# Performance work log

Hardware: AMD Instinct MI355X
Metric: run time of the kernel (lower is better)

The kernel has to match this reference:

```python
import jax, jax.numpy as jnp
import numpy as np


def setup_inputs() -> dict:
    key = jax.random.key(0)
    ks = jax.random.split(key, 6)
    bs, T, F, HS, da, r = 64, 512, 128, 256, 64, 8
    s = 0.05  # xavier-ish scale, keeps gates out of saturation
    return {
        "x": jax.random.normal(ks[0], (bs, T, F), jnp.float32),
        "w_first": jax.random.normal(ks[1], (da, F), jnp.float32) * s,
        "b_first": jnp.zeros((da,), jnp.float32),
        "w_second": jax.random.normal(ks[2], (r, da), jnp.float32) * s,
        "b_second": jnp.zeros((r,), jnp.float32),
        "weight_iBarh": jax.random.normal(ks[3], (F, 4 * HS), jnp.float32) * s,
        "weight_hh": jax.random.normal(ks[4], (HS, 4 * HS), jnp.float32) * s,
        "bias": jnp.zeros((4 * HS,), jnp.float32),
    }


def reference(x, w_first, b_first, w_second, b_second, weight_iBarh, weight_hh, bias):
    bs, T, F = x.shape
    HS = weight_hh.shape[0]
    r = w_second.shape[0]
    # attention scores are a fixed per-position function of x -> precompute once
    scores = jnp.tanh(x @ w_first.T + b_first) @ w_second.T + b_second  # [bs, T, r]
    neg = jnp.finfo(x.dtype).min
    t_idx = jnp.arange(T)

    def step(carry, t):
        h, c = carry
        # growing-window softmax over time axis: positions 0..t
        mask = (t_idx <= t)[None, :, None]  # [1, T, 1]
        attn = jax.nn.softmax(jnp.where(mask, scores, neg), axis=1)  # [bs, T, r]
        # matrixM: attention^T @ pastTimeSteps, summed over r heads / r
        M = jnp.einsum('btr,btf->bf', attn, x) / r  # [bs, F]
        gates = M @ weight_iBarh + h @ weight_hh + bias  # [bs, 4*HS]
        i = jax.nn.sigmoid(gates[:, :HS])
        f = jax.nn.sigmoid(gates[:, HS:2 * HS])
        g = jnp.tanh(gates[:, 2 * HS:3 * HS])
        o = jax.nn.sigmoid(gates[:, 3 * HS:])
        c = f * c + i * g
        h = o * jnp.tanh(c)
        return (h, c), h

    h0 = jnp.zeros((bs, HS), x.dtype)
    c0 = jnp.zeros((bs, HS), x.dtype)
    (h_t, c_t), hs = jax.lax.scan(step, (h0, c0), t_idx)
    hidden_seq = jnp.transpose(hs, (1, 0, 2))  # [bs, T, HS]
    # attention returned by the torch code is from the LAST step (full window)
    attention = jnp.transpose(jax.nn.softmax(scores, axis=1), (0, 2, 1))  # [bs, r, T]
    return hidden_seq, h_t, c_t, attention
```

## Files before the change

### kernel.cpp

```cpp
#include <hip/hip_runtime.h>
#include <cmath>

#define T_LEN 512
#define BS    64
#define F_DIM 128
#define HSZ   256
#define DA    64
#define RH    8

#define OFF_HT   8388608
#define OFF_CT   8404992
#define OFF_ATT  8421376

__global__ __launch_bounds__(256) void k_scores(
    const float* __restrict__ x, const float* __restrict__ w1,
    const float* __restrict__ b1, const float* __restrict__ w2,
    const float* __restrict__ b2, float* __restrict__ scores)
{
  __shared__ float wl[DA * 129];
  __shared__ float xs[4][F_DIM];
  __shared__ float hid[4][DA];
  int tid = threadIdx.x;
  for (int id = tid; id < DA * F_DIM; id += 256) {
    int a = id >> 7, f = id & 127;
    wl[a * 129 + f] = w1[id];
  }
  int wv = tid >> 6, lane = tid & 63;
  int pair = blockIdx.x * 4 + wv;
  const float* xr = x + (size_t)pair * F_DIM;
  xs[wv][lane]      = xr[lane];
  xs[wv][64 + lane] = xr[64 + lane];
  __syncthreads();
  float acc = b1[lane];
  #pragma unroll 8
  for (int f = 0; f < F_DIM; ++f)
    acc += xs[wv][f] * wl[lane * 129 + f];
  hid[wv][lane] = tanhf(acc);
  __syncthreads();
  if (lane < RH) {
    float sc = b2[lane];
    #pragma unroll 8
    for (int a = 0; a < DA; ++a)
      sc += hid[wv][a] * w2[lane * DA + a];
    scores[(size_t)pair * RH + lane] = sc;
  }
}

__global__ __launch_bounds__(512) void k_attn_M(
    const float* __restrict__ x, const float* __restrict__ scores,
    float* __restrict__ M, float* __restrict__ out)
{
  __shared__ float se[T_LEN * 9];
  __shared__ float ivd[T_LEN * 9];
  __shared__ float segsum[RH][65];
  __shared__ float cp[4 * F_DIM * RH];
  __shared__ float gmax[RH];
  int tid = threadIdx.x;
  int blk = blockIdx.x;
  int j = blk >> 6, b = blk & 63;
  int p0 = j * 128, e = p0 + 128;
  int e8 = e * 8;
  const float* sb = scores + (size_t)b * T_LEN * RH;
  for (int id = tid; id < e8; id += 512)
    se[(id >> 3) * 9 + (id & 7)] = sb[id];
  __syncthreads();
  {
    int w = tid >> 6, l = tid & 63;
    float m = -INFINITY;
    for (int t = l; t < e; t += 64)
      m = fmaxf(m, se[t * 9 + w]);
    #pragma unroll
    for (int off = 32; off; off >>= 1)
      m = fmaxf(m, __shfl_xor(m, off));
    if (l == 0) gmax[w] = m;
  }
  __syncthreads();
  for (int id = tid; id < e8; id += 512) {
    int t = id >> 3, r = id & 7;
    se[t * 9 + r] = expf(se[t * 9 + r] - gmax[r]);
  }
  __syncthreads();
  int nseg = e >> 3;
  {
    int r = tid >> 6, seg = tid & 63;
    if (seg < nseg) {
      float run = 0.f;
      #pragma unroll
      for (int i = 0; i < 8; ++i) {
        int t = seg * 8 + i;
        run += se[t * 9 + r];
        ivd[t * 9 + r] = run;
      }
      segsum[r][seg] = run;
    }
  }
  __syncthreads();
  if (tid < RH) {
    float off = 0.f;
    for (int sg = 0; sg < nseg; ++sg) {
      float tmp = segsum[tid][sg];
      segsum[tid][sg] = off;
      off += tmp;
    }
  }
  __syncthreads();
  for (int id = tid; id < e8; id += 512) {
    int t = id >> 3, r = id & 7;
    ivd[t * 9 + r] = 1.f / (ivd[t * 9 + r] + segsum[r][t >> 3]);
  }
  __syncthreads();
  if (j == 3) {
    for (int id = tid; id < T_LEN * RH; id += 512) {
      int r = id >> 9, t = id & 511;
      out[OFF_ATT + ((size_t)b * RH + r) * T_LEN + t] =
          se[t * 9 + r] * ivd[511 * 9 + r];
    }
  }
  const float* xb = x + (size_t)b * T_LEN * F_DIM;
  {
    int q = tid >> 7, f = tid & 127;
    int len = p0 >> 2;
    int t0 = q * len, t1 = t0 + len;
    float pp[RH];
    #pragma unroll
    for (int r = 0; r < RH; ++r) pp[r] = 0.f;
    for (int t = t0; t < t1; ++t) {
      float xv = xb[t * F_DIM + f];
      #pragma unroll
      for (int r = 0; r < RH; ++r) pp[r] += se[t * 9 + r] * xv;
    }
    float* c = &cp[(q * F_DIM + f) * RH];
    #pragma unroll
    for (int r = 0; r < RH; ++r) c[r] = pp[r];
  }
  __syncthreads();
  if (tid < F_DIM) {
    int f = tid;
    float num[RH];
    #pragma unroll
    for (int r = 0; r < RH; ++r) num[r] = 0.f;
    #pragma unroll
    for (int q = 0; q < 4; ++q) {
      const float* c = &cp[(q * F_DIM + f) * RH];
      #pragma unroll
      for (int r = 0; r < RH; ++r) num[r] += c[r];
    }
    float* Mb = M + (size_t)b * T_LEN * F_DIM;
    for (int t = p0; t < e; ++t) {
      float xv = xb[t * F_DIM + f];
      float acc = 0.f;
      #pragma unroll
      for (int r = 0; r < RH; ++r) {
        num[r] += se[t * 9 + r] * xv;
        acc += num[r] * ivd[t * 9 + r];
      }
      Mb[t * F_DIM + f] = 0.125f * acc;
    }
  }
}

__global__ __launch_bounds__(1024, 4) void k_lstm(
    const float* __restrict__ M, const float* __restrict__ Wi,
    const float* __restrict__ Wh, const float* __restrict__ bias,
    unsigned long long* __restrict__ slab64,
    float* __restrict__ out)
{
  __shared__ float v[HSZ];
  __shared__ float mst[F_DIM];
  __shared__ float part[1024];
  int tid = threadIdx.x;
  int blk = blockIdx.x;
  int s = blk >> 6;
  int b = blk & 63;
  int kq = tid >> 8;
  int ct = tid & 255;
  int type = ct >> 6, jj = ct & 63;
  int col = type * 256 + s * 64 + jj;

  float w[96];
  #pragma unroll
  for (int k = 0; k < 96; ++k) {
    int kk = kq * 96 + k;
    w[k] = (kk < F_DIM) ? Wi[(size_t)kk * 1024 + col]
                        : Wh[(size_t)(kk - F_DIM) * 1024 + col];
  }
  float bsum = (kq == 0) ? bias[col] : 0.f;
  float c_reg = 0.f;

  if (tid < HSZ) v[tid] = 0.f;
  if (tid >= 512 && tid < 512 + F_DIM)
    mst[tid - 512] = M[(size_t)b * T_LEN * F_DIM + (tid - 512)];
  __syncthreads();

  int pidx = tid >> 6;
  int sp = pidx + (pidx >= s);
  int pj = tid & 63;

  for (int t = 0; t < T_LEN; ++t) {
    float acc = bsum;
    if (kq == 0) {
      #pragma unroll
      for (int k = 0; k < 96; ++k) acc += mst[k] * w[k];
    } else if (kq == 1) {
      #pragma unroll
      for (int k = 0; k < 32; ++k) acc += mst[96 + k] * w[k];
      #pragma unroll
      for (int k = 32; k < 96; ++k) acc += v[k - 32] * w[k];
    } else if (kq == 2) {
      #pragma unroll
      for (int k = 0; k < 96; ++k) acc += v[64 + k] * w[k];
    } else {
      #pragma unroll
      for (int k = 0; k < 96; ++k) acc += v[160 + k] * w[k];
    }
    part[tid] = acc;
    __syncthreads();

    if (tid < 64) {
      float gi = part[tid]       + part[256 + tid] + part[512 + tid] + part[768 + tid];
      float gf = part[64 + tid]  + part[320 + tid] + part[576 + tid] + part[832 + tid];
      float gg = part[128 + tid] + part[384 + tid] + part[640 + tid] + part[896 + tid];
      float go = part[192 + tid] + part[448 + tid] + part[704 + tid] + part[960 + tid];
      float ii = 1.f / (1.f + __expf(-gi));
      float ff = 1.f / (1.f + __expf(-gf));
      float gt = 1.f - 2.f / (__expf(2.f * gg) + 1.f);
      float oo = 1.f / (1.f + __expf(-go));
      c_reg = ff * c_reg + ii * gt;
      float tc = 1.f - 2.f / (__expf(2.f * c_reg) + 1.f);
      float h = oo * tc;
      int hsx = s * 64 + tid;
      v[hsx] = h;
      unsigned long long pk =
          ((unsigned long long)(unsigned)(t + 1) << 32) |
          (unsigned long long)__float_as_uint(h);
      __hip_atomic_store(&slab64[(((t & 1) * BS + b) * 4 + s) * 64 + tid], pk,
                         __ATOMIC_RELAXED, __HIP_MEMORY_SCOPE_AGENT);
      out[((size_t)b * T_LEN + t) * HSZ + hsx] = h;
      if (t == T_LEN - 1) {
        out[OFF_HT + b * HSZ + hsx] = h;
        out[OFF_CT + b * HSZ + hsx] = c_reg;
      }
    }

    if (t < T_LEN - 1) {
      if (tid >= 512 && tid < 512 + F_DIM)
        mst[tid - 512] = M[((size_t)b * T_LEN + t + 1) * F_DIM + (tid - 512)];
      if (tid < 192) {
        const unsigned long long* addr =
            &slab64[(((t & 1) * BS + b) * 4 + sp) * 64 + pj];
        unsigned want = (unsigned)(t + 1);
        unsigned long long got;
        do {
          got = __hip_atomic_load(addr, __ATOMIC_RELAXED,
                                  __HIP_MEMORY_SCOPE_AGENT);
        } while ((unsigned)(got >> 32) != want);
        v[sp * 64 + pj] = __uint_as_float((unsigned)(got & 0xffffffffu));
      }
      __syncthreads();
    }
  }
}

extern "C" void kernel_launch(void* const* d_in, const int* in_sizes, int n_in,
                              void* d_out, int out_size, void* d_ws, size_t ws_size,
                              hipStream_t stream) {
  const float* x   = (const float*)d_in[0];
  const float* w1  = (const float*)d_in[1];
  const float* b1  = (const float*)d_in[2];
  const float* w2  = (const float*)d_in[3];
  const float* b2  = (const float*)d_in[4];
  const float* Wi  = (const float*)d_in[5];
  const float* Wh  = (const float*)d_in[6];
  const float* bia = (const float*)d_in[7];
  float* out = (float*)d_out;
  float* ws  = (float*)d_ws;

  float* scores = ws;
  float* M      = ws + 262144;
  unsigned long long* slab64 =
      (unsigned long long*)(ws + 262144 + 4194304);

  hipLaunchKernelGGL(k_scores, dim3(8192), dim3(256), 0, stream,
                     x, w1, b1, w2, b2, scores);
  hipLaunchKernelGGL(k_attn_M, dim3(256), dim3(512), 0, stream,
                     x, scores, M, out);
  hipLaunchKernelGGL(k_lstm, dim3(256), dim3(1024), 0, stream,
                     M, Wi, Wh, bia, slab64, out);
}
```

Measured before the change: 1.083 ms.

## Split LSTM across 16 hidden slices with 4 batch rows per block, pipelined

Restructures the recurrent LSTM kernel so each block owns a 16-wide hidden slice for four batch rows instead of a 64-wide slice for one row. The four batch rows are processed in a rotating pipeline, so waiting on peer blocks' h values for one row overlaps with computing gates for another. Per-thread weight registers drop from 96 to 24 and the gate reduction uses wave shuffles. This adds more cross-block spin-waits and two barriers per row-step, and the launch-side grid configuration is not visible here.

```diff
diff --git a/kernel.cpp b/kernel.cpp
--- a/kernel.cpp
+++ b/kernel.cpp
@@ -165,100 +165,112 @@
     unsigned long long* __restrict__ slab64,
     float* __restrict__ out)
 {
-  __shared__ float v[HSZ];
-  __shared__ float mst[F_DIM];
+  __shared__ float u[4][2][384];
   __shared__ float part[1024];
   int tid = threadIdx.x;
   int blk = blockIdx.x;
-  int s = blk >> 6;
-  int b = blk & 63;
-  int kq = tid >> 8;
-  int ct = tid & 255;
-  int type = ct >> 6, jj = ct & 63;
-  int col = type * 256 + s * 64 + jj;
-
-  float w[96];
+  int sl = blk >> 4;
+  int bq = blk & 15;
+  int b0 = bq * 4;
+  int kq = tid >> 6;
+  int col = tid & 63;
+  int hs = col >> 2, type = col & 3;
+  int gcol = type * 256 + sl * 16 + hs;
+
+  float w[24];
   #pragma unroll
-  for (int k = 0; k < 96; ++k) {
-    int kk = kq * 96 + k;
-    w[k] = (kk < F_DIM) ? Wi[(size_t)kk * 1024 + col]
-                        : Wh[(size_t)(kk - F_DIM) * 1024 + col];
-  }
-  float bsum = (kq == 0) ? bias[col] : 0.f;
-  float c_reg = 0.f;
-
-  if (tid < HSZ) v[tid] = 0.f;
-  if (tid >= 512 && tid < 512 + F_DIM)
-    mst[tid - 512] = M[(size_t)b * T_LEN * F_DIM + (tid - 512)];
-  __syncthreads();
-
-  int pidx = tid >> 6;
-  int sp = pidx + (pidx >= s);
-  int pj = tid & 63;
+  for (int i = 0; i < 24; ++i) {
+    int kk = kq * 24 + i;
+    w[i] = (kk < F_DIM) ? Wi[(size_t)kk * 1024 + gcol]
+                        : Wh[(size_t)(kk - F_DIM) * 1024 + gcol];
+  }
+  float bsum = (kq == 0) ? bias[gcol] : 0.f;
+  const float* Mb = M + (size_t)b0 * T_LEN * F_DIM;
+
+  { int q = tid >> 8, idx = tid & 255; u[q][0][128 + idx] = 0.f; }
+  if (tid >= 512) {
+    int r = tid - 512, q = r >> 7, f = r & 127;
+    u[q][0][f] = Mb[((size_t)q * T_LEN) * F_DIM + f];
+  }
+  __syncthreads();
+
+  float cc0 = 0.f, cc1 = 0.f, cc2 = 0.f, cc3 = 0.f;
+  float4 mreg = {0.f, 0.f, 0.f, 0.f};
+
+#define SEG(Q, CREG) do { \
+    int par = t & 1; \
+    if (Q == 0 && tid >= 896) {   \
+      int rr = tid - 896, qs = rr >> 5, f4 = rr & 31; \
+      int ts = (t + 1 < T_LEN) ? t + 1 : 0; \
+      mreg = *(const float4*)&Mb[((size_t)qs * T_LEN + ts) * F_DIM + f4 * 4]; \
+    } \
+    {  \
+      const float* uq = &u[Q][par][kq * 24]; \
+      float acc = bsum; \
+      _Pragma("unroll") \
+      for (int i = 0; i < 24; ++i) acc += uq[i] * w[i]; \
+      part[tid] = acc; \
+    } \
+    if (tid >= 256 && tid < 496) {   \
+      int rr = tid - 256, p = rr >> 4, phs = rr & 15; \
+      int sp = p + (p >= sl); \
+      int Qn = (Q + 1) & 3; \
+      int tau = (Q == 3) ? t + 1 : t; \
+      if (tau >= 1 && tau < T_LEN) { \
+        const unsigned long long* ad = \
+            &slab64[(size_t)(tau & 1) * 16384 + (size_t)(b0 + Qn) * 256 + sp * 16 + phs]; \
+        unsigned long long got; \
+        do { got = __hip_atomic_load(ad, __ATOMIC_RELAXED, __HIP_MEMORY_SCOPE_AGENT); } \
+        while ((unsigned)(got >> 32) != (unsigned)tau); \
+        u[Qn][tau & 1][128 + sp * 16 + phs] = __uint_as_float((unsigned)got); \
+      } \
+    } \
+    __syncthreads(); \
+    if (tid < 256) {   \
+      int colr = tid >> 2, s4 = tid & 3; \
+      float tot = part[(4 * s4 + 0) * 64 + colr] + part[(4 * s4 + 1) * 64 + colr] \
+                + part[(4 * s4 + 2) * 64 + colr] + part[(4 * s4 + 3) * 64 + colr]; \
+      tot += __shfl_xor(tot, 1); \
+      tot += __shfl_xor(tot, 2); \
+      int lane = tid & 63; \
+      float gF = __shfl(tot, (lane + 4) & 63); \
+      float gG = __shfl(tot, (lane + 8) & 63); \
+      float gO = __shfl(tot, (lane + 12) & 63); \
+      if ((tid & 15) == 0) { \
+        int h = tid >> 4; \
+        float ii = 1.f / (1.f + __expf(-tot)); \
+        float ff = 1.f / (1.f + __expf(-gF)); \
+        float gg = 1.f - 2.f / (__expf(2.f * gG) + 1.f); \
+        float oo = 1.f / (1.f + __expf(-gO)); \
+        CREG = ff * CREG + ii * gg; \
+        float tc = 1.f - 2.f / (__expf(2.f * CREG) + 1.f); \
+        float hv = oo * tc; \
+        u[Q][par ^ 1][128 + sl * 16 + h] = hv; \
+        unsigned long long pk = ((unsigned long long)(unsigned)(t + 1) << 32) \
+                              | (unsigned long long)__float_as_uint(hv); \
+        __hip_atomic_store(&slab64[(size_t)(par ^ 1) * 16384 + (size_t)(b0 + Q) * 256 + sl * 16 + h], \
+                           pk, __ATOMIC_RELAXED, __HIP_MEMORY_SCOPE_AGENT); \
+        out[((size_t)(b0 + Q) * T_LEN + t) * HSZ + sl * 16 + h] = hv; \
+        if (t == T_LEN - 1) { \
+          out[OFF_HT + (b0 + Q) * HSZ + sl * 16 + h] = hv; \
+          out[OFF_CT + (b0 + Q) * HSZ + sl * 16 + h] = CREG; \
+        } \
+      } \
+    } \
+    if (Q == 1 && tid >= 896) {   \
+      int rr = tid - 896, qs = rr >> 5, f4 = rr & 31; \
+      if (t + 1 < T_LEN) *(float4*)&u[qs][(t + 1) & 1][f4 * 4] = mreg; \
+    } \
+    __syncthreads(); \
+  } while (0)
 
   for (int t = 0; t < T_LEN; ++t) {
-    float acc = bsum;
-    if (kq == 0) {
-      #pragma unroll
-      for (int k = 0; k < 96; ++k) acc += mst[k] * w[k];
-    } else if (kq == 1) {
-      #pragma unroll
-      for (int k = 0; k < 32; ++k) acc += mst[96 + k] * w[k];
-      #pragma unroll
-      for (int k = 32; k < 96; ++k) acc += v[k - 32] * w[k];
-    } else if (kq == 2) {
-      #pragma unroll
-      for (int k = 0; k < 96; ++k) acc += v[64 + k] * w[k];
-    } else {
-      #pragma unroll
-      for (int k = 0; k < 96; ++k) acc += v[160 + k] * w[k];
-    }
-    part[tid] = acc;
-    __syncthreads();
-
-    if (tid < 64) {
-      float gi = part[tid]       + part[256 + tid] + part[512 + tid] + part[768 + tid];
-      float gf = part[64 + tid]  + part[320 + tid] + part[576 + tid] + part[832 + tid];
-      float gg = part[128 + tid] + part[384 + tid] + part[640 + tid] + part[896 + tid];
-      float go = part[192 + tid] + part[448 + tid] + part[704 + tid] + part[960 + tid];
-      float ii = 1.f / (1.f + __expf(-gi));
-      float ff = 1.f / (1.f + __expf(-gf));
-      float gt = 1.f - 2.f / (__expf(2.f * gg) + 1.f);
-      float oo = 1.f / (1.f + __expf(-go));
-      c_reg = ff * c_reg + ii * gt;
-      float tc = 1.f - 2.f / (__expf(2.f * c_reg) + 1.f);
-      float h = oo * tc;
-      int hsx = s * 64 + tid;
-      v[hsx] = h;
-      unsigned long long pk =
-          ((unsigned long long)(unsigned)(t + 1) << 32) |
-          (unsigned long long)__float_as_uint(h);
-      __hip_atomic_store(&slab64[(((t & 1) * BS + b) * 4 + s) * 64 + tid], pk,
-                         __ATOMIC_RELAXED, __HIP_MEMORY_SCOPE_AGENT);
-      out[((size_t)b * T_LEN + t) * HSZ + hsx] = h;
-      if (t == T_LEN - 1) {
-        out[OFF_HT + b * HSZ + hsx] = h;
-        out[OFF_CT + b * HSZ + hsx] = c_reg;
-      }
-    }
-
-    if (t < T_LEN - 1) {
-      if (tid >= 512 && tid < 512 + F_DIM)
-        mst[tid - 512] = M[((size_t)b * T_LEN + t + 1) * F_DIM + (tid - 512)];
-      if (tid < 192) {
-        const unsigned long long* addr =
-            &slab64[(((t & 1) * BS + b) * 4 + sp) * 64 + pj];
-        unsigned want = (unsigned)(t + 1);
-        unsigned long long got;
-        do {
-          got = __hip_atomic_load(addr, __ATOMIC_RELAXED,
-                                  __HIP_MEMORY_SCOPE_AGENT);
-        } while ((unsigned)(got >> 32) != want);
-        v[sp * 64 + pj] = __uint_as_float((unsigned)(got & 0xffffffffu));
-      }
-      __syncthreads();
-    }
-  }
+    SEG(0, cc0);
+    SEG(1, cc1);
+    SEG(2, cc2);
+    SEG(3, cc3);
+  }
+#undef SEG
 }
 
 extern "C" void kernel_launch(void* const* d_in, const int* in_sizes, int n_in,
```

Result: slower. 2.175 ms (+100.9%).
